# Kernel optimization log

Measured on AMD Instinct MI355X. Metric: run time of the kernel, lower is better.

## Reference

```python
import jax, jax.numpy as jnp
import numpy as np

N_HEAD = 16
N_FEAT = 1024
D_K = N_FEAT // N_HEAD


def rtt_half(x):
    x1, x2 = x[..., : x.shape[-1] // 2], x[..., x.shape[-1] // 2 :]
    return jnp.concatenate([-x2, x1], axis=-1)


def setup_inputs() -> dict:
    key = jax.random.key(0)
    ks = jax.random.split(key, 16)
    B, T, D = 4, 2048, N_FEAT
    inp = {
        "query": jax.random.normal(ks[0], (B, T, D), jnp.float32),
        "key": jax.random.normal(ks[1], (B, T, D), jnp.float32),
        "value": jax.random.normal(ks[2], (B, T, D), jnp.float32),
        "cos": jax.random.uniform(ks[3], (T, 1, D_K), jnp.float32),
        "sin": jax.random.uniform(ks[4], (T, 1, D_K), jnp.float32),
        "mask": jnp.zeros((B, T, T), jnp.bool_),
    }
    s = 1.0 / np.sqrt(D)
    inp["Wq"] = jax.random.uniform(ks[5], (D, D), jnp.float32, -s, s)
    inp["bq"] = jax.random.uniform(ks[6], (D,), jnp.float32, -s, s)
    inp["Wk"] = jax.random.uniform(ks[7], (D, D), jnp.float32, -s, s)
    inp["bk"] = jax.random.uniform(ks[8], (D,), jnp.float32, -s, s)
    inp["Wv"] = jax.random.uniform(ks[9], (D, D), jnp.float32, -s, s)
    inp["bv"] = jax.random.uniform(ks[10], (D,), jnp.float32, -s, s)
    inp["Wo"] = jax.random.uniform(ks[11], (D, D), jnp.float32, -s, s)
    inp["bo"] = jax.random.uniform(ks[12], (D,), jnp.float32, -s, s)
    return inp


def reference(query, key, value, cos, sin, mask, Wq, bq, Wk, bk, Wv, bv, Wo, bo):
    B, T, D = query.shape
    h, d_k = N_HEAD, D_K
    # QKV projections (torch Linear: x @ W.T + b), reshape to (B,T,h,d_k)
    q = (query @ Wq.T + bq).reshape(B, T, h, d_k)
    k = (key @ Wk.T + bk).reshape(B, T, h, d_k)
    v = (value @ Wv.T + bv).reshape(B, T, h, d_k)
    # RoPE: cos/sin sliced to T, broadcast (T,1,d_k) over (B,T,h,d_k)
    c, s = cos[:T], sin[:T]
    q = q * c + rtt_half(q) * s
    k = k * c + rtt_half(k) * s
    # attention scores (B,h,T,T)
    scores = jnp.einsum("bqhd,bkhd->bhqk", q, k) / np.sqrt(d_k).astype(jnp.float32)
    scores = jnp.where(mask[:, None, :, :], -jnp.inf, scores)
    attn = jax.nn.softmax(scores, axis=-1)
    out = jnp.einsum("bhqk,bkhd->bqhd", attn, v).reshape(B, T, D)
    return out @ Wo.T + bo
```

## Files before the change

kernel.cpp:

```cpp
#include <hip/hip_runtime.h>

#define B_SZ 4
#define T_SZ 2048
#define D_SZ 1024
#define H_SZ 16
#define DK_SZ 64
#define M_SZ (B_SZ * T_SZ)

typedef __attribute__((ext_vector_type(8))) short bf16x8;
typedef __attribute__((ext_vector_type(4))) float f32x4;

union fui { float f; unsigned u; };

static __device__ inline short f2bf(float x) {
    union { float f; unsigned u; } v; v.f = x;
    unsigned r = v.u + 0x7fff + ((v.u >> 16) & 1);
    return (short)(r >> 16);
}
static __device__ inline void split1(float f, short* h, short* l) {
    fui a; a.f = f;
    *h = (short)(a.u >> 16);
    fui t; t.u = a.u & 0xffff0000u;
    fui r; r.f = f - t.f;
    *l = (short)(r.u >> 16);
}

#define MFMA16(a, b, c) __builtin_amdgcn_mfma_f32_16x16x32_bf16((a), (b), (c), 0, 0, 0)

#define GLDS16(g, l) __builtin_amdgcn_global_load_lds(                        \
    (const __attribute__((address_space(1))) unsigned int*)(g),               \
    (__attribute__((address_space(3))) unsigned int*)(l), 16, 0, 0)

__global__ __launch_bounds__(256)
void wsplit_kernel(const float* __restrict__ W, short* __restrict__ Wh,
                   short* __restrict__ Wl)
{
    const int i = blockIdx.x * 256 + threadIdx.x;
    float4 f = ((const float4*)W)[i];
    fui a[4]; a[0].f = f.x; a[1].f = f.y; a[2].f = f.z; a[3].f = f.w;
    union { short s[4]; short4 v; } H, L;
#pragma unroll
    for (int j = 0; j < 4; ++j) {
        H.s[j] = (short)(a[j].u >> 16);
        fui t; t.u = a[j].u & 0xffff0000u;
        fui r; r.f = a[j].f - t.f;
        L.s[j] = (short)(r.u >> 16);
    }
    ((short4*)Wh)[i] = H.v;
    ((short4*)Wl)[i] = L.v;
}

__global__ __launch_bounds__(256)
void mask_flags_kernel(const unsigned char* __restrict__ mask, int* __restrict__ flags)
{
    const int f = blockIdx.x * 4 + (threadIdx.x >> 6);
    const int lane = threadIdx.x & 63;
    const int b = f >> 10, qt = (f >> 5) & 31, kt = f & 31;
    const unsigned char* base = mask + ((size_t)b * T_SZ + qt * 64) * T_SZ + kt * 64;
    bool nz = false;
#pragma unroll
    for (int i = 0; i < 4; ++i) {
        const int c = lane + 64 * i;
        const int row = c >> 2, off = (c & 3) * 16;
        uint4 v = *(const uint4*)(base + (size_t)row * T_SZ + off);
        nz |= ((v.x | v.y | v.z | v.w) != 0);
    }
    unsigned long long bal = __ballot(nz);
    if (lane == 0) flags[f] = (bal != 0) ? 1 : 0;
}

__global__ __launch_bounds__(256)
void qkv_mfma_kernel(const short* __restrict__ Ah, const short* __restrict__ Al,
                     const short* __restrict__ Wh, const short* __restrict__ Wl,
                     const float* __restrict__ bias,
                     const float* __restrict__ cosb, const float* __restrict__ sinb,
                     short* __restrict__ Hd, short* __restrict__ Ld,
                     short* __restrict__ Vb, const int which)
{
    __shared__ __align__(16) short Ahs[2][4096];
    __shared__ __align__(16) short Als[2][4096];
    __shared__ __align__(16) short Whs[2][4096];
    __shared__ __align__(16) short Wls[2][4096];

    const int m0 = blockIdx.x * 128, n0 = blockIdx.y * 128;
    const int tid = threadIdx.x;
    const int wv = tid >> 6, lane = tid & 63;
    const int wm = wv >> 1, wn = wv & 1;
    const int l15 = lane & 15, quad = lane >> 4;

    f32x4 acc[4][4];
#pragma unroll
    for (int mt = 0; mt < 4; ++mt)
#pragma unroll
        for (int nt = 0; nt < 4; ++nt)
            acc[mt][nt] = (f32x4){0.f, 0.f, 0.f, 0.f};

    const size_t aoff = (size_t)(m0 + wv * 32 + (lane >> 2)) * D_SZ + (lane & 3) * 8;
    const size_t woff = (size_t)(n0 + wv * 32 + (lane >> 2)) * D_SZ + (lane & 3) * 8;
    const short* ahg = Ah + aoff;
    const short* alg = Al + aoff;
    const short* whg = Wh + woff;
    const short* wlg = Wl + woff;

#define STAGEQ(bi, kk)                                                        \
    do {                                                                      \
        short* a0 = &Ahs[bi][wv * 1024];                                      \
        short* a1 = &Als[bi][wv * 1024];                                      \
        short* w0 = &Whs[bi][wv * 1024];                                      \
        short* w1 = &Wls[bi][wv * 1024];                                      \
        GLDS16(ahg + (kk),             a0);                                   \
        GLDS16(ahg + 16 * D_SZ + (kk), a0 + 512);                             \
        GLDS16(alg + (kk),             a1);                                   \
        GLDS16(alg + 16 * D_SZ + (kk), a1 + 512);                             \
        GLDS16(whg + (kk),             w0);                                   \
        GLDS16(whg + 16 * D_SZ + (kk), w0 + 512);                             \
        GLDS16(wlg + (kk),             w1);                                   \
        GLDS16(wlg + 16 * D_SZ + (kk), w1 + 512);                             \
    } while (0)

    STAGEQ(0, 0);
    for (int k0 = 0; k0 < D_SZ; k0 += 32) {
        const int cur = (k0 >> 5) & 1;
        __syncthreads();
        if (k0 + 32 < D_SZ) STAGEQ(cur ^ 1, k0 + 32);

        bf16x8 ah[4], al[4];
#pragma unroll
        for (int mt = 0; mt < 4; ++mt) {
            const int arow = (wm * 64 + mt * 16 + l15) * 32 + quad * 8;
            ah[mt] = *(const bf16x8*)&Ahs[cur][arow];
            al[mt] = *(const bf16x8*)&Als[cur][arow];
        }
#pragma unroll
        for (int nt = 0; nt < 4; ++nt) {
            const int brow = (wn * 64 + nt * 16 + l15) * 32 + quad * 8;
            const bf16x8 bh = *(const bf16x8*)&Whs[cur][brow];
            const bf16x8 bl = *(const bf16x8*)&Wls[cur][brow];
#pragma unroll
            for (int mt = 0; mt < 4; ++mt) {
                acc[mt][nt] = MFMA16(ah[mt], bh, acc[mt][nt]);
                acc[mt][nt] = MFMA16(al[mt], bh, acc[mt][nt]);
                acc[mt][nt] = MFMA16(ah[mt], bl, acc[mt][nt]);
            }
        }
    }
#undef STAGEQ

    const int hh = (blockIdx.y << 1) + wn;
    if (which < 2) {
        const float qscale = (which == 0) ? 0.125f : 1.0f;
#pragma unroll
        for (int mt = 0; mt < 4; ++mt)
#pragma unroll
            for (int p = 0; p < 2; ++p) {
                const int d1 = p * 16 + l15, d2 = d1 + 32;
                const int col1 = n0 + wn * 64 + d1;
                const float b1 = bias[col1], b2 = bias[col1 + 32];
#pragma unroll
                for (int r = 0; r < 4; ++r) {
                    const int m = m0 + wm * 64 + mt * 16 + quad * 4 + r;
                    const int bb = m >> 11, tg = m & (T_SZ - 1);
                    const float c1 = cosb[tg * 64 + d1], s1 = sinb[tg * 64 + d1];
                    const float c2 = cosb[tg * 64 + d2], s2 = sinb[tg * 64 + d2];
                    const float x1 = acc[mt][p][r] + b1;
                    const float x2 = acc[mt][p + 2][r] + b2;
                    const float y1 = (x1 * c1 - x2 * s1) * qscale;
                    const float y2 = (x2 * c2 + x1 * s2) * qscale;
                    const size_t base = (((size_t)(bb * H_SZ + hh)) * T_SZ + tg) * 64;
                    short h_, l_;
                    split1(y1, &h_, &l_); Hd[base + d1] = h_; Ld[base + d1] = l_;
                    split1(y2, &h_, &l_); Hd[base + d2] = h_; Ld[base + d2] = l_;
                }
            }
    } else {
#pragma unroll
        for (int nt = 0; nt < 4; ++nt) {
            const int d = nt * 16 + l15;
            const float bvv = bias[n0 + wn * 64 + d];
#pragma unroll
            for (int mt = 0; mt < 4; ++mt)
#pragma unroll
                for (int r = 0; r < 4; ++r) {
                    const int m = m0 + wm * 64 + mt * 16 + quad * 4 + r;
                    const int bb = m >> 11, tg = m & (T_SZ - 1);
                    Vb[(((size_t)(bb * H_SZ + hh)) * T_SZ + tg) * 64 + d] =
                        f2bf(acc[mt][nt][r] + bvv);
                }
        }
    }
}

__global__ __launch_bounds__(256)
void gemm_out_kernel(const short* __restrict__ Ah, const short* __restrict__ Al,
                     const short* __restrict__ Wh, const short* __restrict__ Wl,
                     const float* __restrict__ bias, float* __restrict__ C)
{
    __shared__ __align__(16) short Ahs[2][4096];
    __shared__ __align__(16) short Als[2][4096];
    __shared__ __align__(16) short Whs[2][4096];
    __shared__ __align__(16) short Wls[2][4096];

    const int m0 = blockIdx.x * 128, n0 = blockIdx.y * 128;
    const int tid = threadIdx.x;
    const int wv = tid >> 6, lane = tid & 63;
    const int wm = wv >> 1, wn = wv & 1;
    const int l15 = lane & 15, quad = lane >> 4;

    f32x4 acc[4][4];
#pragma unroll
    for (int mt = 0; mt < 4; ++mt)
#pragma unroll
        for (int nt = 0; nt < 4; ++nt)
            acc[mt][nt] = (f32x4){0.f, 0.f, 0.f, 0.f};

    const size_t aoff = (size_t)(m0 + wv * 32 + (lane >> 2)) * D_SZ + (lane & 3) * 8;
    const size_t woff = (size_t)(n0 + wv * 32 + (lane >> 2)) * D_SZ + (lane & 3) * 8;
    const short* ahg = Ah + aoff;
    const short* alg = Al + aoff;
    const short* whg = Wh + woff;
    const short* wlg = Wl + woff;

#define STAGEO(bi, kk)                                                        \
    do {                                                                      \
        short* a0 = &Ahs[bi][wv * 1024];                                      \
        short* a1 = &Als[bi][wv * 1024];                                      \
        short* w0 = &Whs[bi][wv * 1024];                                      \
        short* w1 = &Wls[bi][wv * 1024];                                      \
        GLDS16(ahg + (kk),             a0);                                   \
        GLDS16(ahg + 16 * D_SZ + (kk), a0 + 512);                             \
        GLDS16(alg + (kk),             a1);                                   \
        GLDS16(alg + 16 * D_SZ + (kk), a1 + 512);                             \
        GLDS16(whg + (kk),             w0);                                   \
        GLDS16(whg + 16 * D_SZ + (kk), w0 + 512);                             \
        GLDS16(wlg + (kk),             w1);                                   \
        GLDS16(wlg + 16 * D_SZ + (kk), w1 + 512);                             \
    } while (0)

    STAGEO(0, 0);
    for (int k0 = 0; k0 < D_SZ; k0 += 32) {
        const int cur = (k0 >> 5) & 1;
        __syncthreads();
        if (k0 + 32 < D_SZ) STAGEO(cur ^ 1, k0 + 32);

        bf16x8 ah[4], al[4];
#pragma unroll
        for (int mt = 0; mt < 4; ++mt) {
            const int arow = (wm * 64 + mt * 16 + l15) * 32 + quad * 8;
            ah[mt] = *(const bf16x8*)&Ahs[cur][arow];
            al[mt] = *(const bf16x8*)&Als[cur][arow];
        }
#pragma unroll
        for (int nt = 0; nt < 4; ++nt) {
            const int brow = (wn * 64 + nt * 16 + l15) * 32 + quad * 8;
            const bf16x8 bh = *(const bf16x8*)&Whs[cur][brow];
            const bf16x8 bl = *(const bf16x8*)&Wls[cur][brow];
#pragma unroll
            for (int mt = 0; mt < 4; ++mt) {
                acc[mt][nt] = MFMA16(ah[mt], bh, acc[mt][nt]);
                acc[mt][nt] = MFMA16(al[mt], bh, acc[mt][nt]);
                acc[mt][nt] = MFMA16(ah[mt], bl, acc[mt][nt]);
            }
        }
    }
#undef STAGEO

#pragma unroll
    for (int nt = 0; nt < 4; ++nt) {
        const int col = n0 + wn * 64 + nt * 16 + l15;
        const float bvv = bias[col];
#pragma unroll
        for (int mt = 0; mt < 4; ++mt)
#pragma unroll
            for (int r = 0; r < 4; ++r) {
                const int m = m0 + wm * 64 + mt * 16 + quad * 4 + r;
                C[(size_t)m * D_SZ + col] = acc[mt][nt][r] + bvv;
            }
    }
}

__global__ __launch_bounds__(256, 6)
void attn_mfma_kernel(const short* __restrict__ Qhg, const short* __restrict__ Qlg,
                      const short* __restrict__ Khg, const short* __restrict__ Klg,
                      const short* __restrict__ Vg,
                      const unsigned char* __restrict__ mask,
                      const int* __restrict__ flags,
                      short* __restrict__ Oh, short* __restrict__ Ol)
{
    __shared__ __align__(16) short Khs[64 * 72];
    __shared__ __align__(16) short Kls[64 * 72];
    __shared__ __align__(16) short Vt[64 * 72];
    __shared__ __align__(16) short Ps[4 * 16 * 72];

    const int bh = blockIdx.y;
    const int b = bh >> 4, h = bh & 15;
    const int q0 = blockIdx.x * 64;
    const int tid = threadIdx.x;
    const int wv = tid >> 6, lane = tid & 63;
    const int l15 = lane & 15, quad = lane >> 4;

    const short* qhp = Qhg + ((size_t)bh * T_SZ + q0 + wv * 16 + l15) * 64 + quad * 8;
    const short* qlp = Qlg + ((size_t)bh * T_SZ + q0 + wv * 16 + l15) * 64 + quad * 8;
    bf16x8 qh[2], ql[2];
#pragma unroll
    for (int s = 0; s < 2; ++s) {
        qh[s] = *(const bf16x8*)(qhp + 32 * s);
        ql[s] = *(const bf16x8*)(qlp + 32 * s);
    }

    f32x4 accO[4];
#pragma unroll
    for (int nt = 0; nt < 4; ++nt) accO[nt] = (f32x4){0.f, 0.f, 0.f, 0.f};
    float m_i[4], l_i[4];
#pragma unroll
    for (int r = 0; r < 4; ++r) { m_i[r] = -1e30f; l_i[r] = 0.f; }

    const short* khb = Khg + (size_t)bh * T_SZ * 64;
    const short* klb = Klg + (size_t)bh * T_SZ * 64;
    const short* vb  = Vg  + (size_t)bh * T_SZ * 64;
    const unsigned char* mbase = mask + ((size_t)b * T_SZ + q0) * T_SZ;
    const int* frow = flags + ((size_t)b * 32 + blockIdx.x) * 32;

    const short* kgp[4];
    short*       kld[4];
#pragma unroll
    for (int jj = 0; jj < 4; ++jj) {
        const int cc = tid + 256 * (jj & 1);
        const int row = cc >> 3, off = (cc & 7) * 8;
        kgp[jj] = ((jj < 2) ? khb : klb) + (size_t)row * 64 + off;
        kld[jj] = ((jj < 2) ? Khs : Kls) + row * 72 + off;
    }
    const int vt0 = (tid & 15) * 4, vd0 = (tid >> 4) * 4;
    const short* vgp[4];
#pragma unroll
    for (int i = 0; i < 4; ++i)
        vgp[i] = vb + (size_t)(vt0 + i) * 64 + vd0;
    short* pw = &Ps[wv * 16 * 72];

    bf16x8 kst[4];
    uint2  rv[4];
#pragma unroll
    for (int jj = 0; jj < 4; ++jj) kst[jj] = *(const bf16x8*)(kgp[jj]);
#pragma unroll
    for (int i = 0; i < 4; ++i)    rv[i]   = *(const uint2*)(vgp[i]);

    for (int kti = 0; kti < 32; ++kti) {
        const int kt = kti * 64;
        __syncthreads();
#pragma unroll
        for (int jj = 0; jj < 4; ++jj)
            *(bf16x8*)kld[jj] = kst[jj];
#pragma unroll
        for (int c = 0; c < 4; ++c) {
            const int k = c >> 1;
            const unsigned sel = (c & 1) ? 0x07060302u : 0x05040100u;
            const unsigned lo0 = k ? rv[0].y : rv[0].x;
            const unsigned lo1 = k ? rv[1].y : rv[1].x;
            const unsigned lo2 = k ? rv[2].y : rv[2].x;
            const unsigned lo3 = k ? rv[3].y : rv[3].x;
            uint2 o;
            o.x = __builtin_amdgcn_perm(lo1, lo0, sel);
            o.y = __builtin_amdgcn_perm(lo3, lo2, sel);
            *(uint2*)&Vt[(vd0 + c) * 72 + vt0] = o;
        }
        if (kti < 31) {
            const size_t adv = (size_t)(kt + 64) * 64;
#pragma unroll
            for (int jj = 0; jj < 4; ++jj)
                kst[jj] = *(const bf16x8*)(kgp[jj] + adv);
#pragma unroll
            for (int i = 0; i < 4; ++i)
                rv[i] = *(const uint2*)(vgp[i] + adv);
        }
        __syncthreads();

        f32x4 accS[4];
        __builtin_amdgcn_s_setprio(1);
#pragma unroll
        for (int nt = 0; nt < 4; ++nt) {
            f32x4 acc = (f32x4){0.f, 0.f, 0.f, 0.f};
#pragma unroll
            for (int s = 0; s < 2; ++s) {
                const bf16x8 kh = *(const bf16x8*)&Khs[(nt * 16 + l15) * 72 + 32 * s + quad * 8];
                const bf16x8 kl = *(const bf16x8*)&Kls[(nt * 16 + l15) * 72 + 32 * s + quad * 8];
                acc = MFMA16(qh[s], kh, acc);
                acc = MFMA16(ql[s], kh, acc);
                acc = MFMA16(qh[s], kl, acc);
            }
            accS[nt] = acc;
        }
        __builtin_amdgcn_s_setprio(0);

        float sv[4][4];
        if (frow[kti]) {
#pragma unroll
            for (int nt = 0; nt < 4; ++nt)
#pragma unroll
                for (int r = 0; r < 4; ++r) {
                    const unsigned char mb =
                        mbase[(size_t)(wv * 16 + quad * 4 + r) * T_SZ + kt + nt * 16 + l15];
                    sv[nt][r] = mb ? -1e30f : accS[nt][r];
                }
        } else {
#pragma unroll
            for (int nt = 0; nt < 4; ++nt)
#pragma unroll
                for (int r = 0; r < 4; ++r)
                    sv[nt][r] = accS[nt][r];
        }

        float rmax[4];
#pragma unroll
        for (int r = 0; r < 4; ++r)
            rmax[r] = fmaxf(fmaxf(sv[0][r], sv[1][r]), fmaxf(sv[2][r], sv[3][r]));
#pragma unroll
        for (int off = 1; off < 16; off <<= 1)
#pragma unroll
            for (int r = 0; r < 4; ++r)
                rmax[r] = fmaxf(rmax[r], __shfl_xor(rmax[r], off, 64));

        float alpha[4];
#pragma unroll
        for (int r = 0; r < 4; ++r) {
            const float mnew = fmaxf(m_i[r], rmax[r]);
            alpha[r] = __expf(m_i[r] - mnew);
            m_i[r] = mnew;
        }
        float lsum[4] = {0.f, 0.f, 0.f, 0.f};
#pragma unroll
        for (int nt = 0; nt < 4; ++nt)
#pragma unroll
            for (int r = 0; r < 4; ++r) {
                const float p = __expf(sv[nt][r] - m_i[r]);
                sv[nt][r] = p;
                lsum[r] += p;
            }
#pragma unroll
        for (int r = 0; r < 4; ++r)
            l_i[r] = l_i[r] * alpha[r] + lsum[r];

#pragma unroll
        for (int nt = 0; nt < 4; ++nt)
#pragma unroll
            for (int r = 0; r < 4; ++r) {
                fui u; u.f = sv[nt][r];
                pw[(quad * 4 + r) * 72 + nt * 16 + l15] = (short)((u.u + 0x8000u) >> 16);
            }

#pragma unroll
        for (int nt = 0; nt < 4; ++nt)
#pragma unroll
            for (int r = 0; r < 4; ++r)
                accO[nt][r] *= alpha[r];

        bf16x8 pa[2];
#pragma unroll
        for (int s = 0; s < 2; ++s)
            pa[s] = *(const bf16x8*)&pw[l15 * 72 + 32 * s + quad * 8];
        __builtin_amdgcn_s_setprio(1);
#pragma unroll
        for (int nt = 0; nt < 4; ++nt)
#pragma unroll
            for (int s = 0; s < 2; ++s) {
                const bf16x8 vf = *(const bf16x8*)&Vt[(nt * 16 + l15) * 72 + 32 * s + quad * 8];
                accO[nt] = MFMA16(pa[s], vf, accO[nt]);
            }
        __builtin_amdgcn_s_setprio(0);
    }

#pragma unroll
    for (int off = 1; off < 16; off <<= 1)
#pragma unroll
        for (int r = 0; r < 4; ++r)
            l_i[r] += __shfl_xor(l_i[r], off, 64);

#pragma unroll
    for (int r = 0; r < 4; ++r) {
        const float inv = 1.f / l_i[r];
        const int t = q0 + wv * 16 + quad * 4 + r;
        const size_t base = ((size_t)(b * T_SZ + t)) * D_SZ + h * DK_SZ;
#pragma unroll
        for (int nt = 0; nt < 4; ++nt) {
            short h_, l_;
            split1(accO[nt][r] * inv, &h_, &l_);
            Oh[base + nt * 16 + l15] = h_;
            Ol[base + nt * 16 + l15] = l_;
        }
    }
}

extern "C" void kernel_launch(void* const* d_in, const int* in_sizes, int n_in,
                              void* d_out, int out_size, void* d_ws, size_t ws_size,
                              hipStream_t stream)
{
    const float* query = (const float*)d_in[0];
    const float* key   = (const float*)d_in[1];
    const float* value = (const float*)d_in[2];
    const float* cosb  = (const float*)d_in[3];
    const float* sinb  = (const float*)d_in[4];
    const unsigned char* mask = (const unsigned char*)d_in[5];
    const float* Wq = (const float*)d_in[6];
    const float* bq = (const float*)d_in[7];
    const float* Wk = (const float*)d_in[8];
    const float* bk = (const float*)d_in[9];
    const float* Wv = (const float*)d_in[10];
    const float* bv = (const float*)d_in[11];
    const float* Wo = (const float*)d_in[12];
    const float* bo = (const float*)d_in[13];
    float* out = (float*)d_out;

    short* sp = (short*)d_ws;
    const size_t eb = (size_t)B_SZ * H_SZ * T_SZ * DK_SZ;
    short* Qh = sp;          short* Ql = sp + eb;
    short* Kh = sp + 2 * eb; short* Kl = sp + 3 * eb;
    short* Vb = sp + 4 * eb;
    short* Xh = sp + 5 * eb; short* Xl = sp + 6 * eb;
    short* wsp = sp + 7 * eb;
    const size_t wlen = (size_t)D_SZ * D_SZ;
    short* wqh = wsp;            short* wql = wsp + wlen;
    short* wkh = wsp + 2 * wlen; short* wkl = wsp + 3 * wlen;
    short* wvh = wsp + 4 * wlen; short* wvl = wsp + 5 * wlen;
    short* woh = wsp + 6 * wlen; short* wol = wsp + 7 * wlen;
    int* flags = (int*)(wsp + 8 * wlen);

    const int wsBlocks = (int)(wlen / 4 / 256);
    const int aBlocks  = (int)((size_t)M_SZ * D_SZ / 4 / 256);
    wsplit_kernel<<<wsBlocks, 256, 0, stream>>>(Wq, wqh, wql);
    wsplit_kernel<<<wsBlocks, 256, 0, stream>>>(Wk, wkh, wkl);
    wsplit_kernel<<<wsBlocks, 256, 0, stream>>>(Wv, wvh, wvl);
    wsplit_kernel<<<wsBlocks, 256, 0, stream>>>(Wo, woh, wol);

    mask_flags_kernel<<<1024, 256, 0, stream>>>(mask, flags);

    wsplit_kernel<<<aBlocks, 256, 0, stream>>>(query, Xh, Xl);
    qkv_mfma_kernel<<<dim3(M_SZ / 128, 8), 256, 0, stream>>>(
        Xh, Xl, wqh, wql, bq, cosb, sinb, Qh, Ql, Vb, 0);
    wsplit_kernel<<<aBlocks, 256, 0, stream>>>(key, Xh, Xl);
    qkv_mfma_kernel<<<dim3(M_SZ / 128, 8), 256, 0, stream>>>(
        Xh, Xl, wkh, wkl, bk, cosb, sinb, Kh, Kl, Vb, 1);
    wsplit_kernel<<<aBlocks, 256, 0, stream>>>(value, Xh, Xl);
    qkv_mfma_kernel<<<dim3(M_SZ / 128, 8), 256, 0, stream>>>(
        Xh, Xl, wvh, wvl, bv, cosb, sinb, Qh, Ql, Vb, 2);

    attn_mfma_kernel<<<dim3(T_SZ / 64, B_SZ * H_SZ), 256, 0, stream>>>(
        Qh, Ql, Kh, Kl, Vb, mask, flags, Xh, Xl);

    gemm_out_kernel<<<dim3(M_SZ / 128, D_SZ / 128), 256, 0, stream>>>(
        Xh, Xl, woh, wol, bo, out);
}
```

Before: 656.9 us.

## Double attention query tile to 128 rows with 8 waves sharing K/V tiles

```diff
diff --git a/kernel.cpp b/kernel.cpp
--- a/kernel.cpp
+++ b/kernel.cpp
@@ -278,7 +278,7 @@
     }
 }
 
-__global__ __launch_bounds__(256, 6)
+__global__ __launch_bounds__(512, 6)
 void attn_mfma_kernel(const short* __restrict__ Qhg, const short* __restrict__ Qlg,
                       const short* __restrict__ Khg, const short* __restrict__ Klg,
                       const short* __restrict__ Vg,
@@ -289,11 +289,11 @@
     __shared__ __align__(16) short Khs[64 * 72];
     __shared__ __align__(16) short Kls[64 * 72];
     __shared__ __align__(16) short Vt[64 * 72];
-    __shared__ __align__(16) short Ps[4 * 16 * 72];
+    __shared__ __align__(16) short Ps[8 * 16 * 72];
 
     const int bh = blockIdx.y;
     const int b = bh >> 4, h = bh & 15;
-    const int q0 = blockIdx.x * 64;
+    const int q0 = blockIdx.x * 128;
     const int tid = threadIdx.x;
     const int wv = tid >> 6, lane = tid & 63;
     const int l15 = lane & 15, quad = lane >> 4;
@@ -318,18 +318,24 @@
     const short* klb = Klg + (size_t)bh * T_SZ * 64;
     const short* vb  = Vg  + (size_t)bh * T_SZ * 64;
     const unsigned char* mbase = mask + ((size_t)b * T_SZ + q0) * T_SZ;
-    const int* frow = flags + ((size_t)b * 32 + blockIdx.x) * 32;
-
-    const short* kgp[4];
-    short*       kld[4];
-#pragma unroll
-    for (int jj = 0; jj < 4; ++jj) {
-        const int cc = tid + 256 * (jj & 1);
+    const int* frow = flags + ((size_t)b * 32 + blockIdx.x * 2 + (wv >> 2)) * 32;
+
+    const bool krole = (tid < 256);
+    const int  stid  = tid & 255;
+
+    const short* kgp[2];
+    short*       kldh[2];
+    short*       kldl[2];
+#pragma unroll
+    for (int jj = 0; jj < 2; ++jj) {
+        const int cc = stid + 256 * jj;
         const int row = cc >> 3, off = (cc & 7) * 8;
-        kgp[jj] = ((jj < 2) ? khb : klb) + (size_t)row * 64 + off;
-        kld[jj] = ((jj < 2) ? Khs : Kls) + row * 72 + off;
-    }
-    const int vt0 = (tid & 15) * 4, vd0 = (tid >> 4) * 4;
+        kgp[jj]  = khb + (size_t)row * 64 + off;
+        kldh[jj] = Khs + row * 72 + off;
+        kldl[jj] = Kls + row * 72 + off;
+    }
+    const ptrdiff_t lodiff = klb - khb;
+    const int vt0 = (stid & 15) * 4, vd0 = (stid >> 4) * 4;
     const short* vgp[4];
 #pragma unroll
     for (int i = 0; i < 4; ++i)
@@ -338,38 +344,54 @@
 
     bf16x8 kst[4];
     uint2  rv[4];
-#pragma unroll
-    for (int jj = 0; jj < 4; ++jj) kst[jj] = *(const bf16x8*)(kgp[jj]);
-#pragma unroll
-    for (int i = 0; i < 4; ++i)    rv[i]   = *(const uint2*)(vgp[i]);
+    if (krole) {
+#pragma unroll
+        for (int jj = 0; jj < 2; ++jj) {
+            kst[jj]     = *(const bf16x8*)(kgp[jj]);
+            kst[jj + 2] = *(const bf16x8*)(kgp[jj] + lodiff);
+        }
+    } else {
+#pragma unroll
+        for (int i = 0; i < 4; ++i) rv[i] = *(const uint2*)(vgp[i]);
+    }
 
     for (int kti = 0; kti < 32; ++kti) {
         const int kt = kti * 64;
         __syncthreads();
-#pragma unroll
-        for (int jj = 0; jj < 4; ++jj)
-            *(bf16x8*)kld[jj] = kst[jj];
-#pragma unroll
-        for (int c = 0; c < 4; ++c) {
-            const int k = c >> 1;
-            const unsigned sel = (c & 1) ? 0x07060302u : 0x05040100u;
-            const unsigned lo0 = k ? rv[0].y : rv[0].x;
-            const unsigned lo1 = k ? rv[1].y : rv[1].x;
-            const unsigned lo2 = k ? rv[2].y : rv[2].x;
-            const unsigned lo3 = k ? rv[3].y : rv[3].x;
-            uint2 o;
-            o.x = __builtin_amdgcn_perm(lo1, lo0, sel);
-            o.y = __builtin_amdgcn_perm(lo3, lo2, sel);
-            *(uint2*)&Vt[(vd0 + c) * 72 + vt0] = o;
+        if (krole) {
+#pragma unroll
+            for (int jj = 0; jj < 2; ++jj) {
+                *(bf16x8*)kldh[jj] = kst[jj];
+                *(bf16x8*)kldl[jj] = kst[jj + 2];
+            }
+        } else {
+#pragma unroll
+            for (int c = 0; c < 4; ++c) {
+                const int k = c >> 1;
+                const unsigned sel = (c & 1) ? 0x07060302u : 0x05040100u;
+                const unsigned lo0 = k ? rv[0].y : rv[0].x;
+                const unsigned lo1 = k ? rv[1].y : rv[1].x;
+                const unsigned lo2 = k ? rv[2].y : rv[2].x;
+                const unsigned lo3 = k ? rv[3].y : rv[3].x;
+                uint2 o;
+                o.x = __builtin_amdgcn_perm(lo1, lo0, sel);
+                o.y = __builtin_amdgcn_perm(lo3, lo2, sel);
+                *(uint2*)&Vt[(vd0 + c) * 72 + vt0] = o;
+            }
         }
         if (kti < 31) {
             const size_t adv = (size_t)(kt + 64) * 64;
-#pragma unroll
-            for (int jj = 0; jj < 4; ++jj)
-                kst[jj] = *(const bf16x8*)(kgp[jj] + adv);
-#pragma unroll
-            for (int i = 0; i < 4; ++i)
-                rv[i] = *(const uint2*)(vgp[i] + adv);
+            if (krole) {
+#pragma unroll
+                for (int jj = 0; jj < 2; ++jj) {
+                    kst[jj]     = *(const bf16x8*)(kgp[jj] + adv);
+                    kst[jj + 2] = *(const bf16x8*)(kgp[jj] + lodiff + adv);
+                }
+            } else {
+#pragma unroll
+                for (int i = 0; i < 4; ++i)
+                    rv[i] = *(const uint2*)(vgp[i] + adv);
+            }
         }
         __syncthreads();
 
@@ -541,7 +563,7 @@
     qkv_mfma_kernel<<<dim3(M_SZ / 128, 8), 256, 0, stream>>>(
         Xh, Xl, wvh, wvl, bv, cosb, sinb, Qh, Ql, Vb, 2);
 
-    attn_mfma_kernel<<<dim3(T_SZ / 64, B_SZ * H_SZ), 256, 0, stream>>>(
+    attn_mfma_kernel<<<dim3(T_SZ / 128, B_SZ * H_SZ), 512, 0, stream>>>(
         Qh, Ql, Kh, Kl, Vb, mask, flags, Xh, Xl);
 
     gemm_out_kernel<<<dim3(M_SZ / 128, D_SZ / 128), 256, 0, stream>>>(
```

Result: slower. 940.7 us (+43.2%).

## Merge weight/query split and mask-flag kernels; reuse K LDS for P tile

Applied to the files above, without the earlier changes.

```diff
diff --git a/kernel.cpp b/kernel.cpp
--- a/kernel.cpp
+++ b/kernel.cpp
@@ -31,12 +31,8 @@
     (const __attribute__((address_space(1))) unsigned int*)(g),               \
     (__attribute__((address_space(3))) unsigned int*)(l), 16, 0, 0)
 
-__global__ __launch_bounds__(256)
-void wsplit_kernel(const float* __restrict__ W, short* __restrict__ Wh,
-                   short* __restrict__ Wl)
-{
-    const int i = blockIdx.x * 256 + threadIdx.x;
-    float4 f = ((const float4*)W)[i];
+static __device__ inline void split4_store(const float4 f, short4* Hp, short4* Lp)
+{
     fui a[4]; a[0].f = f.x; a[1].f = f.y; a[2].f = f.z; a[3].f = f.w;
     union { short s[4]; short4 v; } H, L;
 #pragma unroll
@@ -46,27 +42,53 @@
         fui r; r.f = a[j].f - t.f;
         L.s[j] = (short)(r.u >> 16);
     }
-    ((short4*)Wh)[i] = H.v;
-    ((short4*)Wl)[i] = L.v;
+    *Hp = H.v; *Lp = L.v;
 }
 
 __global__ __launch_bounds__(256)
-void mask_flags_kernel(const unsigned char* __restrict__ mask, int* __restrict__ flags)
-{
-    const int f = blockIdx.x * 4 + (threadIdx.x >> 6);
-    const int lane = threadIdx.x & 63;
-    const int b = f >> 10, qt = (f >> 5) & 31, kt = f & 31;
-    const unsigned char* base = mask + ((size_t)b * T_SZ + qt * 64) * T_SZ + kt * 64;
-    bool nz = false;
-#pragma unroll
-    for (int i = 0; i < 4; ++i) {
-        const int c = lane + 64 * i;
-        const int row = c >> 2, off = (c & 3) * 16;
-        uint4 v = *(const uint4*)(base + (size_t)row * T_SZ + off);
-        nz |= ((v.x | v.y | v.z | v.w) != 0);
-    }
-    unsigned long long bal = __ballot(nz);
-    if (lane == 0) flags[f] = (bal != 0) ? 1 : 0;
+void wsplit_kernel(const float* __restrict__ W, short* __restrict__ Wh,
+                   short* __restrict__ Wl)
+{
+    const size_t i = (size_t)blockIdx.x * 256 + threadIdx.x;
+    split4_store(((const float4*)W)[i], &((short4*)Wh)[i], &((short4*)Wl)[i]);
+}
+
+__global__ __launch_bounds__(256)
+void preproc_kernel(const float* __restrict__ W0, const float* __restrict__ W1,
+                    const float* __restrict__ W2, const float* __restrict__ W3,
+                    const float* __restrict__ query,
+                    short* __restrict__ Whd, short* __restrict__ Wld,
+                    short* __restrict__ Xh, short* __restrict__ Xl,
+                    const unsigned char* __restrict__ mask, int* __restrict__ flags)
+{
+    const int bid = blockIdx.x;
+    const int tid = threadIdx.x;
+    if (bid < 4096) {
+        const int which = bid >> 10;
+        const float* W = (which == 0) ? W0 : (which == 1) ? W1 : (which == 2) ? W2 : W3;
+        const size_t i = (size_t)(bid & 1023) * 256 + tid;
+        short* Hd = Whd + (size_t)which * 2 * D_SZ * D_SZ;
+        short* Ld = Wld + (size_t)which * 2 * D_SZ * D_SZ;
+        split4_store(((const float4*)W)[i], &((short4*)Hd)[i], &((short4*)Ld)[i]);
+    } else if (bid < 12288) {
+        const size_t i = (size_t)(bid - 4096) * 256 + tid;
+        split4_store(((const float4*)query)[i], &((short4*)Xh)[i], &((short4*)Xl)[i]);
+    } else {
+        const int f = (bid - 12288) * 4 + (tid >> 6);
+        const int lane = tid & 63;
+        const int b = f >> 10, qt = (f >> 5) & 31, kt = f & 31;
+        const unsigned char* base = mask + ((size_t)b * T_SZ + qt * 64) * T_SZ + kt * 64;
+        bool nz = false;
+#pragma unroll
+        for (int i2 = 0; i2 < 4; ++i2) {
+            const int c = lane + 64 * i2;
+            const int row = c >> 2, off = (c & 3) * 16;
+            uint4 v = *(const uint4*)(base + (size_t)row * T_SZ + off);
+            nz |= ((v.x | v.y | v.z | v.w) != 0);
+        }
+        unsigned long long bal = __ballot(nz);
+        if (lane == 0) flags[f] = (bal != 0) ? 1 : 0;
+    }
 }
 
 __global__ __launch_bounds__(256)
@@ -289,7 +311,6 @@
     __shared__ __align__(16) short Khs[64 * 72];
     __shared__ __align__(16) short Kls[64 * 72];
     __shared__ __align__(16) short Vt[64 * 72];
-    __shared__ __align__(16) short Ps[4 * 16 * 72];
 
     const int bh = blockIdx.y;
     const int b = bh >> 4, h = bh & 15;
@@ -334,7 +355,7 @@
 #pragma unroll
     for (int i = 0; i < 4; ++i)
         vgp[i] = vb + (size_t)(vt0 + i) * 64 + vd0;
-    short* pw = &Ps[wv * 16 * 72];
+    short* pw = &Khs[wv * 16 * 72];
 
     bf16x8 kst[4];
     uint2  rv[4];
@@ -437,6 +458,8 @@
 #pragma unroll
         for (int r = 0; r < 4; ++r)
             l_i[r] = l_i[r] * alpha[r] + lsum[r];
+
+        __syncthreads();
 
 #pragma unroll
         for (int nt = 0; nt < 4; ++nt)
@@ -522,16 +545,10 @@
     short* woh = wsp + 6 * wlen; short* wol = wsp + 7 * wlen;
     int* flags = (int*)(wsp + 8 * wlen);
 
-    const int wsBlocks = (int)(wlen / 4 / 256);
-    const int aBlocks  = (int)((size_t)M_SZ * D_SZ / 4 / 256);
-    wsplit_kernel<<<wsBlocks, 256, 0, stream>>>(Wq, wqh, wql);
-    wsplit_kernel<<<wsBlocks, 256, 0, stream>>>(Wk, wkh, wkl);
-    wsplit_kernel<<<wsBlocks, 256, 0, stream>>>(Wv, wvh, wvl);
-    wsplit_kernel<<<wsBlocks, 256, 0, stream>>>(Wo, woh, wol);
-
-    mask_flags_kernel<<<1024, 256, 0, stream>>>(mask, flags);
-
-    wsplit_kernel<<<aBlocks, 256, 0, stream>>>(query, Xh, Xl);
+    const int aBlocks = (int)((size_t)M_SZ * D_SZ / 4 / 256);
+    preproc_kernel<<<4096 + 8192 + 1024, 256, 0, stream>>>(
+        Wq, Wk, Wv, Wo, query, wqh, wql, Xh, Xl, mask, flags);
+
     qkv_mfma_kernel<<<dim3(M_SZ / 128, 8), 256, 0, stream>>>(
         Xh, Xl, wqh, wql, bq, cosb, sinb, Qh, Ql, Vb, 0);
     wsplit_kernel<<<aBlocks, 256, 0, stream>>>(key, Xh, Xl);
```

Result: no change. 646.0 us, median of 3 (-1.7%).
